# Kernel tuning notes

Hardware: AMD Instinct MI355X
Metric: run time of the kernel (lower is better)

## Reference

```python
import jax, jax.numpy as jnp
import numpy as np

N_ATOMS = 10000
N_EDGES = 150000
NB = 128          # n_atom_basis
NI = 3            # n_interactions
MAX_Z = 100
N_RBF = 20
CUTOFF = 5.0
EPS = 1e-08
BATCH = 64


def setup_inputs() -> dict:
    key = jax.random.key(0)
    ks = jax.random.split(key, 20)
    f32 = jnp.float32
    s = 0.05
    positions = jax.random.normal(ks[0], (N_ATOMS, 3), f32)
    atomic_numbers = jax.random.randint(ks[1], (N_ATOMS,), 0, MAX_Z)
    idx_i = jax.random.randint(ks[2], (N_EDGES,), 0, N_ATOMS)
    off = jax.random.randint(ks[3], (N_EDGES,), 1, N_ATOMS)
    idx_j = (idx_i + off) % N_ATOMS  # avoid self-edges (d_ij == 0)
    idx_m = jnp.sort(jax.random.randint(ks[4], (N_ATOMS,), 0, BATCH))
    emb = (jax.random.normal(ks[5], (MAX_Z, NB), f32) * s).at[0].set(0.0)  # padding_idx=0
    fW = jax.random.normal(ks[6], (N_RBF, NI * 3 * NB), f32) * s
    fb = jnp.zeros((NI * 3 * NB,), f32)
    ic1_W = jax.random.normal(ks[7], (NI, NB, NB), f32) * s
    ic1_b = jnp.zeros((NI, NB), f32)
    ic2_W = jax.random.normal(ks[8], (NI, NB, 3 * NB), f32) * s
    ic2_b = jnp.zeros((NI, 3 * NB), f32)
    mix_W = jax.random.normal(ks[9], (NI, NB, 2 * NB), f32) * s  # no bias
    ctx1_W = jax.random.normal(ks[10], (NI, 2 * NB, NB), f32) * s
    ctx1_b = jnp.zeros((NI, NB), f32)
    ctx2_W = jax.random.normal(ks[11], (NI, NB, 3 * NB), f32) * s
    ctx2_b = jnp.zeros((NI, 3 * NB), f32)
    o1_W = jax.random.normal(ks[12], (NB, NB), f32) * s
    o1_b = jnp.zeros((NB,), f32)
    o2_W = jax.random.normal(ks[13], (NB, NB), f32) * s
    o2_b = jnp.zeros((NB,), f32)
    o3_W = jax.random.normal(ks[14], (NB, 1), f32) * s
    o3_b = jnp.zeros((1,), f32)
    return dict(positions=positions, emb=emb, fW=fW, fb=fb,
                ic1_W=ic1_W, ic1_b=ic1_b, ic2_W=ic2_W, ic2_b=ic2_b,
                mix_W=mix_W, ctx1_W=ctx1_W, ctx1_b=ctx1_b, ctx2_W=ctx2_W, ctx2_b=ctx2_b,
                o1_W=o1_W, o1_b=o1_b, o2_W=o2_W, o2_b=o2_b, o3_W=o3_W, o3_b=o3_b,
                atomic_numbers=atomic_numbers, idx_i=idx_i, idx_j=idx_j, idx_m=idx_m,
                batch_num=BATCH)


def reference(positions, emb, fW, fb, ic1_W, ic1_b, ic2_W, ic2_b,
              mix_W, ctx1_W, ctx1_b, ctx2_W, ctx2_b,
              o1_W, o1_b, o2_W, o2_b, o3_W, o3_b,
              atomic_numbers, idx_i, idx_j, idx_m, batch_num):
    seg = jax.ops.segment_sum
    n_atoms = positions.shape[0]
    # pairwise distances
    r_ij = positions[idx_j] - positions[idx_i]                      # [E,3]
    d_ij = jnp.sqrt(jnp.sum(r_ij * r_ij, axis=-1, keepdims=True))   # [E,1]
    # Gaussian RBF
    offsets = jnp.linspace(0.0, CUTOFF, N_RBF, dtype=positions.dtype)
    width = offsets[1] - offsets[0]
    coeff = -0.5 / (width * width)
    phi = jnp.exp(coeff * (d_ij[..., None] - offsets) ** 2)         # [E,1,20]
    # cosine cutoff
    fcut = (0.5 * (jnp.cos(d_ij * jnp.pi / CUTOFF) + 1.0) * (d_ij < CUTOFF))[..., None]  # [E,1,1]
    filters = (phi @ fW + fb) * fcut                                # [E,1,NI*3*NB]
    dir_ij = r_ij / d_ij                                            # [E,3]
    q = emb[atomic_numbers][:, None]                                # [N,1,NB]
    mu = jnp.zeros((n_atoms, 3, NB), q.dtype)
    for i in range(NI):
        Wij = filters[..., i * 3 * NB:(i + 1) * 3 * NB]             # [E,1,3*NB]
        # interaction
        x = jax.nn.silu(q @ ic1_W[i] + ic1_b[i]) @ ic2_W[i] + ic2_b[i]  # [N,1,3*NB]
        x = Wij * x[idx_j]                                          # [E,1,3*NB]
        dq, dmuR, dmumu = jnp.split(x, 3, axis=-1)                  # [E,1,NB] each
        dq = seg(dq, idx_i, num_segments=n_atoms)                   # [N,1,NB]
        muj = mu[idx_j]                                             # [E,3,NB]
        dmu = dmuR * dir_ij[:, :, None] + dmumu * muj               # [E,3,NB]
        dmu = seg(dmu, idx_i, num_segments=n_atoms)                 # [N,3,NB]
        q = q + dq
        mu = mu + dmu
        # mixing
        mu_mix = mu @ mix_W[i]                                      # [N,3,2*NB]
        mu_V, mu_Wc = jnp.split(mu_mix, 2, axis=-1)                 # [N,3,NB]
        mu_Vn = jnp.sqrt(jnp.sum(mu_V * mu_V, axis=-2, keepdims=True) + EPS)  # [N,1,NB]
        ctx = jnp.concatenate([q, mu_Vn], axis=-1)                  # [N,1,2*NB]
        x = jax.nn.silu(ctx @ ctx1_W[i] + ctx1_b[i]) @ ctx2_W[i] + ctx2_b[i]  # [N,1,3*NB]
        dq_in, dmu_in, dqmu_in = jnp.split(x, 3, axis=-1)
        dmu_in = dmu_in * mu_Wc                                     # [N,3,NB]
        dqmu_in = dqmu_in * jnp.sum(mu_V * mu_Wc, axis=1, keepdims=True)  # [N,1,NB]
        q = q + dq_in + dqmu_in
        mu = mu + dmu_in
    qf = q[:, 0]                                                    # [N,NB]
    h = jax.nn.silu(qf @ o1_W + o1_b)
    h = jax.nn.silu(h @ o2_W + o2_b)
    y = h @ o3_W + o3_b                                             # [N,1]
    y = seg(y, idx_m, num_segments=batch_num)                       # [B,1]
    return (y, mu)
```

## Files before the change

kernel.cpp:

```cpp
#include <hip/hip_runtime.h>
#include <math.h>

#define NA 10000
#define NE 150000
#define NRBF 20
#define CUT 5.0f
#define EPSV 1e-8f
#define NBATCH 64
#define CAP 48
#define PI_F 3.14159265358979323846f

typedef short bf16x8 __attribute__((ext_vector_type(8)));
typedef float f32x4 __attribute__((ext_vector_type(4)));
typedef __fp16 h16x2 __attribute__((ext_vector_type(2)));
typedef unsigned short u16;

__device__ __forceinline__ u16 f2b(float x) {
    unsigned u = __builtin_bit_cast(unsigned, x);
    return (u16)((u + 0x7FFFu + ((u >> 16) & 1u)) >> 16);
}
__device__ __forceinline__ float b2f(u16 b) {
    unsigned u = ((unsigned)b) << 16;
    return __builtin_bit_cast(float, u);
}
__device__ __forceinline__ float silu_f(float x) { return x / (1.0f + expf(-x)); }

#define P_IC1 0
#define P_IC2 49152
#define P_MIX 196608
#define P_C1  294912
#define P_C2  393216
#define P_O1  540672
#define P_O2  557056
#define P_TOT 573440

__global__ __launch_bounds__(64) void pack_k(
    const float* __restrict__ ic1W, const float* __restrict__ ic2W,
    const float* __restrict__ mixW, const float* __restrict__ c1W,
    const float* __restrict__ c2W, const float* __restrict__ o1W,
    const float* __restrict__ o2W, u16* __restrict__ packs) {
    int id = blockIdx.x;
    const float* src; u16* dst; int N, rel;
    if (id < 96)        { int m = id / 32;          rel = id % 32; src = ic1W + m * 16384; dst = packs + P_IC1 + m * 16384; N = 128; }
    else if (id < 384)  { id -= 96;  int m = id / 96; rel = id % 96; src = ic2W + m * 49152; dst = packs + P_IC2 + m * 49152; N = 384; }
    else if (id < 576)  { id -= 384; int m = id / 64; rel = id % 64; src = mixW + m * 32768; dst = packs + P_MIX + m * 32768; N = 256; }
    else if (id < 768)  { id -= 576; int m = id / 64; rel = id % 64; src = c1W  + m * 32768; dst = packs + P_C1  + m * 32768; N = 128; }
    else if (id < 1056) { id -= 768; int m = id / 96; rel = id % 96; src = c2W  + m * 49152; dst = packs + P_C2  + m * 49152; N = 384; }
    else if (id < 1088) { rel = id - 1056; src = o1W; dst = packs + P_O1; N = 128; }
    else                { rel = id - 1088; src = o2W; dst = packs + P_O2; N = 128; }
    int NBT = N >> 4;
    int kb = rel / NBT, nb = rel % NBT;
    int l = threadIdx.x;
    int col = nb * 16 + (l & 15);
    int k0 = kb * 32 + 8 * (l >> 4);
    u16 v[8];
    #pragma unroll
    for (int i = 0; i < 8; i++) v[i] = f2b(src[(size_t)(k0 + i) * N + col]);
    *(bf16x8*)(dst + rel * 512 + l * 8) = *(bf16x8*)v;
}

template<int MT, int K>
__device__ __forceinline__ void stageA(const float* __restrict__ src, int row0,
                                       int maxrow, u16* As) {
    const int NV = MT * K / 4;
    for (int idx = threadIdx.x; idx < NV; idx += 256) {
        int r = idx / (K / 4), c4 = idx % (K / 4);
        float4 v = make_float4(0.f, 0.f, 0.f, 0.f);
        if (row0 + r < maxrow) v = *(const float4*)(src + (size_t)(row0 + r) * K + c4 * 4);
        uint2 o;
        o.x = (unsigned)f2b(v.x) | ((unsigned)f2b(v.y) << 16);
        o.y = (unsigned)f2b(v.z) | ((unsigned)f2b(v.w) << 16);
        *(uint2*)(As + r * (K + 8) + c4 * 4) = o;
    }
}

__device__ __forceinline__ bf16x8 aFrag(const u16* As, int stride, int row, int k0) {
    return *(const bf16x8*)(As + row * stride + k0);
}
__device__ __forceinline__ bf16x8 bFrag(const u16* __restrict__ pack, int NBT,
                                        int ks, int nb, int l) {
    return *(const bf16x8*)(pack + ((size_t)(ks * NBT + nb) * 64 + l) * 8);
}
#define MFMA(a, b, c) __builtin_amdgcn_mfma_f32_16x16x32_bf16(a, b, c, 0, 0, 0)

__global__ void init_q_k(const float* __restrict__ emb, const int* __restrict__ z,
                         float* __restrict__ q) {
    int idx = blockIdx.x * blockDim.x + threadIdx.x;
    if (idx >= NA * 128) return;
    int a = idx >> 7, c = idx & 127;
    q[idx] = emb[z[a] * 128 + c];
}

__global__ void edge_geom_k(const float* __restrict__ pos,
                            const int* __restrict__ idx_i, const int* __restrict__ idx_j,
                            float* __restrict__ edata, int* __restrict__ cnt,
                            int* __restrict__ bucketj) {
    int e = blockIdx.x * blockDim.x + threadIdx.x;
    if (e >= NE) return;
    int i = idx_i[e], j = idx_j[e];
    float rx = pos[j * 3 + 0] - pos[i * 3 + 0];
    float ry = pos[j * 3 + 1] - pos[i * 3 + 1];
    float rz = pos[j * 3 + 2] - pos[i * 3 + 2];
    float d = sqrtf(rx * rx + ry * ry + rz * rz);
    float inv = 1.0f / d;
    float fc = (d < CUT) ? 0.5f * (cosf(d * PI_F / CUT) + 1.0f) : 0.0f;
    const float width = CUT / (float)(NRBF - 1);
    const float coeff = -0.5f / (width * width);
    float ph[NRBF];
    #pragma unroll
    for (int k = 0; k < NRBF; k++) {
        float t = d - (float)k * width;
        ph[k] = expf(coeff * t * t);
    }
    int slot = atomicAdd(&cnt[i], 1);
    if (slot < CAP) {
        bucketj[i * CAP + slot] = j;
        float* ed = edata + ((size_t)i * CAP + slot) * 16;
        ed[0] = rx * inv; ed[1] = ry * inv; ed[2] = rz * inv; ed[3] = fc;
        h16x2* php = (h16x2*)(ed + 4);
        #pragma unroll
        for (int p = 0; p < 10; p++)
            php[p] = __builtin_amdgcn_cvt_pkrtz(ph[2 * p], ph[2 * p + 1]);
    }
}

__global__ void pad_k(int* __restrict__ cnt, int* __restrict__ bucketj,
                      float* __restrict__ edata) {
    int a = blockIdx.x * blockDim.x + threadIdx.x;
    if (a >= NA) return;
    int n = cnt[a]; if (n > CAP) n = CAP;
    int n4 = (n + 3) & ~3;
    for (int k = n; k < n4; k++) {
        bucketj[a * CAP + k] = 0;
        float* ed = edata + ((size_t)a * CAP + k) * 16;
        #pragma unroll
        for (int t = 0; t < 16; t++) ed[t] = 0.f;
    }
    cnt[a] = n4;
}

__global__ __launch_bounds__(256) void mlp1_k(
    const float* __restrict__ q, const u16* __restrict__ pW1, const float* __restrict__ b1,
    const u16* __restrict__ pW2, const float* __restrict__ b2, u16* __restrict__ xmu) {
    __shared__ u16 As[32 * 136];
    __shared__ u16 Hs[32 * 136];
    int abase = blockIdx.x * 32;
    stageA<32, 128>(q, abase, NA, As);
    __syncthreads();
    int l = threadIdx.x & 63, w = threadIdx.x >> 6, lm = l & 15, lg = l >> 4;
    f32x4 acc[2][2];
    #pragma unroll
    for (int j = 0; j < 2; j++)
        #pragma unroll
        for (int mi = 0; mi < 2; mi++) acc[j][mi] = (f32x4){0.f, 0.f, 0.f, 0.f};
    #pragma unroll
    for (int ks = 0; ks < 4; ks++) {
        bf16x8 a0 = aFrag(As, 136, lm, ks * 32 + 8 * lg);
        bf16x8 a1 = aFrag(As, 136, 16 + lm, ks * 32 + 8 * lg);
        #pragma unroll
        for (int j = 0; j < 2; j++) {
            bf16x8 b = bFrag(pW1, 8, ks, w + 4 * j, l);
            acc[j][0] = MFMA(a0, b, acc[j][0]);
            acc[j][1] = MFMA(a1, b, acc[j][1]);
        }
    }
    #pragma unroll
    for (int j = 0; j < 2; j++) {
        int col = 16 * (w + 4 * j) + lm;
        float bb = b1[col];
        #pragma unroll
        for (int mi = 0; mi < 2; mi++)
            #pragma unroll
            for (int v = 0; v < 4; v++)
                Hs[(16 * mi + 4 * lg + v) * 136 + col] = f2b(silu_f(acc[j][mi][v] + bb));
    }
    __syncthreads();
    f32x4 acc2[6][2];
    #pragma unroll
    for (int j = 0; j < 6; j++)
        #pragma unroll
        for (int mi = 0; mi < 2; mi++) acc2[j][mi] = (f32x4){0.f, 0.f, 0.f, 0.f};
    #pragma unroll
    for (int ks = 0; ks < 4; ks++) {
        bf16x8 a0 = aFrag(Hs, 136, lm, ks * 32 + 8 * lg);
        bf16x8 a1 = aFrag(Hs, 136, 16 + lm, ks * 32 + 8 * lg);
        #pragma unroll
        for (int j = 0; j < 6; j++) {
            bf16x8 b = bFrag(pW2, 24, ks, w + 4 * j, l);
            acc2[j][0] = MFMA(a0, b, acc2[j][0]);
            acc2[j][1] = MFMA(a1, b, acc2[j][1]);
        }
    }
    int b = 16 * w + lm;
    #pragma unroll
    for (int mi = 0; mi < 2; mi++)
        #pragma unroll
        for (int v = 0; v < 4; v++) {
            int ga = abase + 16 * mi + 4 * lg + v;
            if (ga >= NA) continue;
            #pragma unroll
            for (int half = 0; half < 2; half++) {
                int c = b + 64 * half;
                float x0 = acc2[half][mi][v]     + b2[c];
                float x1 = acc2[2 + half][mi][v] + b2[128 + c];
                float x2 = acc2[4 + half][mi][v] + b2[256 + c];
                u16* xr = xmu + ((size_t)ga * 128 + c) * 6;
                *(unsigned*)xr = (unsigned)f2b(x0) | ((unsigned)f2b(x1) << 16);
                xr[2] = f2b(x2);
            }
        }
}

template<int IT0>
__global__ __launch_bounds__(128) void gather_k(
    const float* __restrict__ fW, const float* __restrict__ fb,
    const u16* __restrict__ xmu,
    const float* __restrict__ edata, const int* __restrict__ cnt,
    const int* __restrict__ bucketj, int it,
    float* __restrict__ q, float* __restrict__ muF) {
    int a = blockIdx.x;
    int c = threadIdx.x;
    int cb = it * 384;
    h16x2 wp0[10], wp1[10], wp2[10];
    #pragma unroll
    for (int p = 0; p < 10; p++) {
        const float* r0 = fW + (2 * p) * 1152 + cb;
        const float* r1 = fW + (2 * p + 1) * 1152 + cb;
        wp0[p] = __builtin_amdgcn_cvt_pkrtz(r0[c], r1[c]);
        wp1[p] = __builtin_amdgcn_cvt_pkrtz(r0[128 + c], r1[128 + c]);
        if (!IT0) wp2[p] = __builtin_amdgcn_cvt_pkrtz(r0[256 + c], r1[256 + c]);
    }
    float fb0 = fb[cb + c], fb1 = fb[cb + 128 + c];
    float fb2 = IT0 ? 0.f : fb[cb + 256 + c];
    int n4 = cnt[a];
    const int* bj = bucketj + a * CAP;
    const float* eb = edata + (size_t)a * CAP * 16;
    float adq = 0.f, am0 = 0.f, am1 = 0.f, am2 = 0.f;
    for (int e0 = 0; e0 < n4; e0 += 4) {
        int4 j4 = *(const int4*)(bj + e0);
        #pragma unroll
        for (int u = 0; u < 4; u++) {
            int j = __builtin_amdgcn_readfirstlane(
                u == 0 ? j4.x : u == 1 ? j4.y : u == 2 ? j4.z : j4.w);
            const float* ed = eb + (size_t)(e0 + u) * 16;
            const u16* xr = xmu + ((size_t)j * 128 + c) * 6;
            float xc0, xc1, xc2 = 0.f, m0 = 0.f, m1 = 0.f, m2 = 0.f;
            if (IT0) {
                unsigned xv = *(const unsigned*)xr;
                xc0 = b2f((u16)(xv & 0xffff)); xc1 = b2f((u16)(xv >> 16));
            } else {
                uint3 xv = *(const uint3*)xr;
                xc0 = b2f((u16)(xv.x & 0xffff)); xc1 = b2f((u16)(xv.x >> 16));
                xc2 = b2f((u16)(xv.y & 0xffff));
                m0 = b2f((u16)(xv.y >> 16));
                m1 = b2f((u16)(xv.z & 0xffff)); m2 = b2f((u16)(xv.z >> 16));
            }
            float4 gg = *(const float4*)ed;
            const h16x2* php = (const h16x2*)(ed + 4);
            float f0 = fb0, f1 = fb1, f2 = fb2;
            #pragma unroll
            for (int p = 0; p < 10; p++) {
                h16x2 ph = php[p];
                f0 = __builtin_amdgcn_fdot2(ph, wp0[p], f0, false);
                f1 = __builtin_amdgcn_fdot2(ph, wp1[p], f1, false);
                if (!IT0) f2 = __builtin_amdgcn_fdot2(ph, wp2[p], f2, false);
            }
            f0 *= gg.w; f1 *= gg.w;
            float x0 = f0 * xc0, x1 = f1 * xc1;
            adq += x0;
            am0 += x1 * gg.x;
            am1 += x1 * gg.y;
            am2 += x1 * gg.z;
            if (!IT0) {
                f2 *= gg.w;
                float x2 = f2 * xc2;
                am0 += x2 * m0; am1 += x2 * m1; am2 += x2 * m2;
            }
        }
    }
    q[(size_t)a * 128 + c] += adq;
    muF[(size_t)a * 384 + c] += am0;
    muF[(size_t)a * 384 + 128 + c] += am1;
    muF[(size_t)a * 384 + 256 + c] += am2;
}

__global__ __launch_bounds__(256) void mixctx_k(
    float* __restrict__ q, float* __restrict__ muF, u16* __restrict__ xmu,
    const u16* __restrict__ pM,
    const u16* __restrict__ pC1, const float* __restrict__ c1b,
    const u16* __restrict__ pC2, const float* __restrict__ c2b) {
    __shared__ u16 As[48 * 136];
    __shared__ u16 mmL[16 * 768];
    __shared__ u16 Cs[16 * 264];
    __shared__ u16 Hs[16 * 136];
    int abase = blockIdx.x * 16;
    stageA<48, 128>(muF, abase * 3, 3 * NA, As);
    __syncthreads();
    int l = threadIdx.x & 63, w = threadIdx.x >> 6, lm = l & 15, lg = l >> 4;
    {
        f32x4 acc[4][3];
        #pragma unroll
        for (int j = 0; j < 4; j++)
            #pragma unroll
            for (int mi = 0; mi < 3; mi++) acc[j][mi] = (f32x4){0.f, 0.f, 0.f, 0.f};
        #pragma unroll
        for (int ks = 0; ks < 4; ks++) {
            bf16x8 a[3];
            #pragma unroll
            for (int mi = 0; mi < 3; mi++) a[mi] = aFrag(As, 136, 16 * mi + lm, ks * 32 + 8 * lg);
            #pragma unroll
            for (int j = 0; j < 4; j++) {
                bf16x8 b = bFrag(pM, 16, ks, w + 4 * j, l);
                #pragma unroll
                for (int mi = 0; mi < 3; mi++) acc[j][mi] = MFMA(a[mi], b, acc[j][mi]);
            }
        }
        #pragma unroll
        for (int j = 0; j < 4; j++) {
            int col = 16 * (w + 4 * j) + lm;
            #pragma unroll
            for (int mi = 0; mi < 3; mi++)
                #pragma unroll
                for (int v = 0; v < 4; v++) {
                    int R = 16 * mi + 4 * lg + v;
                    mmL[(R / 3) * 768 + (R % 3) * 256 + col] = f2b(acc[j][mi][v]);
                }
        }
    }
    __syncthreads();
    for (int idx = threadIdx.x; idx < 16 * 128; idx += 256) {
        int a = idx >> 7, cc = idx & 127;
        int ga = abase + a;
        float s = EPSV;
        #pragma unroll
        for (int d = 0; d < 3; d++) {
            float t = b2f(mmL[a * 768 + d * 256 + cc]);
            s += t * t;
        }
        float qv = (ga < NA) ? q[(size_t)ga * 128 + cc] : 0.f;
        Cs[a * 264 + cc] = f2b(qv);
        Cs[a * 264 + 128 + cc] = f2b(sqrtf(s));
    }
    __syncthreads();
    {
        f32x4 h[2];
        h[0] = (f32x4){0.f, 0.f, 0.f, 0.f}; h[1] = (f32x4){0.f, 0.f, 0.f, 0.f};
        #pragma unroll
        for (int ks = 0; ks < 8; ks++) {
            bf16x8 a0 = aFrag(Cs, 264, lm, ks * 32 + 8 * lg);
            #pragma unroll
            for (int j = 0; j < 2; j++) {
                bf16x8 b = bFrag(pC1, 8, ks, w + 4 * j, l);
                h[j] = MFMA(a0, b, h[j]);
            }
        }
        #pragma unroll
        for (int j = 0; j < 2; j++) {
            int col = 16 * (w + 4 * j) + lm;
            float bb = c1b[col];
            #pragma unroll
            for (int v = 0; v < 4; v++)
                Hs[(4 * lg + v) * 136 + col] = f2b(silu_f(h[j][v] + bb));
        }
    }
    __syncthreads();
    f32x4 acc2[6];
    #pragma unroll
    for (int j = 0; j < 6; j++) acc2[j] = (f32x4){0.f, 0.f, 0.f, 0.f};
    #pragma unroll
    for (int ks = 0; ks < 4; ks++) {
        bf16x8 a0 = aFrag(Hs, 136, lm, ks * 32 + 8 * lg);
        #pragma unroll
        for (int j = 0; j < 6; j++) {
            bf16x8 b = bFrag(pC2, 24, ks, w + 4 * j, l);
            acc2[j] = MFMA(a0, b, acc2[j]);
        }
    }
    #pragma unroll
    for (int j = 0; j < 6; j++) {
        float bb = c2b[16 * (w + 4 * j) + lm];
        #pragma unroll
        for (int v = 0; v < 4; v++) acc2[j][v] += bb;
    }
    #pragma unroll
    for (int v = 0; v < 4; v++) {
        int al = 4 * lg + v;
        int ga = abase + al;
        if (ga >= NA) continue;
        #pragma unroll
        for (int jj = 0; jj < 2; jj++) {
            int cc = 16 * w + 64 * jj + lm;
            float x0 = acc2[jj][v], x1 = acc2[jj + 2][v], x2 = acc2[jj + 4][v];
            float dot = 0.f, muW[3], mnew[3];
            #pragma unroll
            for (int d = 0; d < 3; d++) {
                float muV = b2f(mmL[al * 768 + d * 256 + cc]);
                muW[d] = b2f(mmL[al * 768 + d * 256 + 128 + cc]);
                dot += muV * muW[d];
            }
            q[(size_t)ga * 128 + cc] += x0 + x2 * dot;
            #pragma unroll
            for (int d = 0; d < 3; d++) {
                size_t mo = (size_t)ga * 384 + d * 128 + cc;
                float m = muF[mo] + x1 * muW[d];
                muF[mo] = m;
                mnew[d] = m;
            }
            u16* xr = xmu + ((size_t)ga * 128 + cc) * 6;
            xr[3] = f2b(mnew[0]);
            *(unsigned*)(xr + 4) = (unsigned)f2b(mnew[1]) | ((unsigned)f2b(mnew[2]) << 16);
        }
    }
}

__global__ __launch_bounds__(256) void readout_k(
    const float* __restrict__ q, const u16* __restrict__ pO1, const float* __restrict__ o1b,
    const u16* __restrict__ pO2, const float* __restrict__ o2b,
    const float* __restrict__ o3W, const float* __restrict__ o3b,
    const int* __restrict__ idx_m, float* __restrict__ y) {
    __shared__ u16 As[32 * 136];
    __shared__ u16 Hs[32 * 136];
    __shared__ float red[256];
    __shared__ float part[NBATCH];
    __shared__ int mlo, mhi;
    int abase = blockIdx.x * 32;
    stageA<32, 128>(q, abase, NA, As);
    __syncthreads();
    int l = threadIdx.x & 63, w = threadIdx.x >> 6, lm = l & 15, lg = l >> 4;
    f32x4 acc[2][2];
    #pragma unroll
    for (int j = 0; j < 2; j++)
        #pragma unroll
        for (int mi = 0; mi < 2; mi++) acc[j][mi] = (f32x4){0.f, 0.f, 0.f, 0.f};
    #pragma unroll
    for (int ks = 0; ks < 4; ks++) {
        bf16x8 a0 = aFrag(As, 136, lm, ks * 32 + 8 * lg);
        bf16x8 a1 = aFrag(As, 136, 16 + lm, ks * 32 + 8 * lg);
        #pragma unroll
        for (int j = 0; j < 2; j++) {
            bf16x8 b = bFrag(pO1, 8, ks, w + 4 * j, l);
            acc[j][0] = MFMA(a0, b, acc[j][0]);
            acc[j][1] = MFMA(a1, b, acc[j][1]);
        }
    }
    #pragma unroll
    for (int j = 0; j < 2; j++) {
        int col = 16 * (w + 4 * j) + lm;
        float bb = o1b[col];
        #pragma unroll
        for (int mi = 0; mi < 2; mi++)
            #pragma unroll
            for (int v = 0; v < 4; v++)
                Hs[(16 * mi + 4 * lg + v) * 136 + col] = f2b(silu_f(acc[j][mi][v] + bb));
    }
    __syncthreads();
    f32x4 acc2[2][2];
    #pragma unroll
    for (int j = 0; j < 2; j++)
        #pragma unroll
        for (int mi = 0; mi < 2; mi++) acc2[j][mi] = (f32x4){0.f, 0.f, 0.f, 0.f};
    #pragma unroll
    for (int ks = 0; ks < 4; ks++) {
        bf16x8 a0 = aFrag(Hs, 136, lm, ks * 32 + 8 * lg);
        bf16x8 a1 = aFrag(Hs, 136, 16 + lm, ks * 32 + 8 * lg);
        #pragma unroll
        for (int j = 0; j < 2; j++) {
            bf16x8 b = bFrag(pO2, 8, ks, w + 4 * j, l);
            acc2[j][0] = MFMA(a0, b, acc2[j][0]);
            acc2[j][1] = MFMA(a1, b, acc2[j][1]);
        }
    }
    #pragma unroll
    for (int j = 0; j < 2; j++) {
        int col = 16 * (w + 4 * j) + lm;
        float bb = o2b[col];
        #pragma unroll
        for (int mi = 0; mi < 2; mi++)
            #pragma unroll
            for (int v = 0; v < 4; v++)
                As[(16 * mi + 4 * lg + v) * 136 + col] = f2b(silu_f(acc2[j][mi][v] + bb));
    }
    if (threadIdx.x < NBATCH) part[threadIdx.x] = 0.f;
    if (threadIdx.x == 0) { mlo = NBATCH; mhi = -1; }
    __syncthreads();
    int a = threadIdx.x >> 3, gseg = threadIdx.x & 7;
    float p = 0.f;
    #pragma unroll
    for (int cc = 0; cc < 16; cc++) {
        int c = gseg * 16 + cc;
        p += b2f(As[a * 136 + c]) * o3W[c];
    }
    red[threadIdx.x] = p;
    __syncthreads();
    if (gseg == 0) {
        float s = 0.f;
        #pragma unroll
        for (int k = 0; k < 8; k++) s += red[a * 8 + k];
        int ga = abase + a;
        if (ga < NA) {
            int m = idx_m[ga];
            atomicAdd(&part[m], s + o3b[0]);
            atomicMin(&mlo, m);
            atomicMax(&mhi, m);
        }
    }
    __syncthreads();
    for (int m = mlo + (int)threadIdx.x; m <= mhi; m += 256)
        atomicAdd(&y[m], part[m]);
}

extern "C" void kernel_launch(void* const* d_in, const int* in_sizes, int n_in,
                              void* d_out, int out_size, void* d_ws, size_t ws_size,
                              hipStream_t stream) {
    const float* pos  = (const float*)d_in[0];
    const float* emb  = (const float*)d_in[1];
    const float* fW   = (const float*)d_in[2];
    const float* fb   = (const float*)d_in[3];
    const float* ic1W = (const float*)d_in[4];
    const float* ic1b = (const float*)d_in[5];
    const float* ic2W = (const float*)d_in[6];
    const float* ic2b = (const float*)d_in[7];
    const float* mixW = (const float*)d_in[8];
    const float* c1W  = (const float*)d_in[9];
    const float* c1b  = (const float*)d_in[10];
    const float* c2W  = (const float*)d_in[11];
    const float* c2b  = (const float*)d_in[12];
    const float* o1W  = (const float*)d_in[13];
    const float* o1b  = (const float*)d_in[14];
    const float* o2W  = (const float*)d_in[15];
    const float* o2b  = (const float*)d_in[16];
    const float* o3W  = (const float*)d_in[17];
    const float* o3b  = (const float*)d_in[18];
    const int* zn     = (const int*)d_in[19];
    const int* idx_i  = (const int*)d_in[20];
    const int* idx_j  = (const int*)d_in[21];
    const int* idx_m  = (const int*)d_in[22];

    float* y   = (float*)d_out;
    float* muF = (float*)d_out + NBATCH;

    char* wp = (char*)d_ws;
    float* q      = (float*)wp;  wp += (size_t)NA * 128 * 4;
    u16*   xmu    = (u16*)wp;    wp += (size_t)NA * 128 * 6 * 2;
    float* edata  = (float*)wp;  wp += (size_t)NA * CAP * 16 * 4;
    int*   cnt    = (int*)wp;    wp += (size_t)NA * 4;
    int*   bucketj= (int*)wp;    wp += (size_t)NA * CAP * 4;
    u16*   packs  = (u16*)wp;    wp += (size_t)P_TOT * 2;

    hipMemsetAsync(d_out, 0, (size_t)(NBATCH + (size_t)NA * 384) * 4, stream);
    hipMemsetAsync(cnt, 0, (size_t)NA * 4, stream);

    pack_k<<<1120, 64, 0, stream>>>(ic1W, ic2W, mixW, c1W, c2W, o1W, o2W, packs);
    init_q_k<<<(NA * 128 + 255) / 256, 256, 0, stream>>>(emb, zn, q);
    edge_geom_k<<<(NE + 255) / 256, 256, 0, stream>>>(pos, idx_i, idx_j, edata, cnt, bucketj);
    pad_k<<<(NA + 255) / 256, 256, 0, stream>>>(cnt, bucketj, edata);

    for (int it = 0; it < 3; it++) {
        mlp1_k<<<313, 256, 0, stream>>>(
            q, packs + P_IC1 + it * 16384, ic1b + it * 128,
            packs + P_IC2 + it * 49152, ic2b + it * 384, xmu);
        if (it == 0)
            gather_k<1><<<NA, 128, 0, stream>>>(
                fW, fb, xmu, edata, cnt, bucketj, it, q, muF);
        else
            gather_k<0><<<NA, 128, 0, stream>>>(
                fW, fb, xmu, edata, cnt, bucketj, it, q, muF);
        mixctx_k<<<(NA + 15) / 16, 256, 0, stream>>>(
            q, muF, xmu,
            packs + P_MIX + it * 32768,
            packs + P_C1 + it * 32768, c1b + it * 128,
            packs + P_C2 + it * 49152, c2b + it * 384);
    }

    readout_k<<<313, 256, 0, stream>>>(q, packs + P_O1, o1b, packs + P_O2, o2b,
                                       o3W, o3b, idx_m, y);
}
```

Measured before the change: 395.9 us.

## Fuse next-iteration interaction MLP into mixctx kernel and prepack filter weights as fp16

The mixing/context kernel now also runs the next iteration's interaction MLP (ic1/ic2) on the freshly updated q held in shared memory. This removes two separate mlp1 launches and a reload of q from global memory. The filter weights fW are also converted once to packed fp16 pairs in pack_k, so gather_k loads pre-converted halves instead of converting per block. The cost is extra shared memory and registers in the fused kernel, which may lower occupancy.

Measured after the change: 407.6 us. 3.0% more time.

```diff
diff --git a/kernel.cpp b/kernel.cpp
--- a/kernel.cpp
+++ b/kernel.cpp
@@ -32,14 +32,27 @@
 #define P_C2  393216
 #define P_O1  540672
 #define P_O2  557056
-#define P_TOT 573440
+#define P_FWH 573440
+#define P_TOT 596480
 
 __global__ __launch_bounds__(64) void pack_k(
     const float* __restrict__ ic1W, const float* __restrict__ ic2W,
     const float* __restrict__ mixW, const float* __restrict__ c1W,
     const float* __restrict__ c2W, const float* __restrict__ o1W,
-    const float* __restrict__ o2W, u16* __restrict__ packs) {
+    const float* __restrict__ o2W, const float* __restrict__ fW,
+    u16* __restrict__ packs) {
     int id = blockIdx.x;
+    if (id >= 1120) {
+        int col = (id - 1120) * 64 + (int)threadIdx.x;
+        unsigned* dst32 = (unsigned*)(packs + P_FWH);
+        #pragma unroll
+        for (int p = 0; p < 10; p++) {
+            h16x2 v = __builtin_amdgcn_cvt_pkrtz(fW[(size_t)(2 * p) * 1152 + col],
+                                                 fW[(size_t)(2 * p + 1) * 1152 + col]);
+            dst32[p * 1152 + col] = __builtin_bit_cast(unsigned, v);
+        }
+        return;
+    }
     const float* src; u16* dst; int N, rel;
     if (id < 96)        { int m = id / 32;          rel = id % 32; src = ic1W + m * 16384; dst = packs + P_IC1 + m * 16384; N = 128; }
     else if (id < 384)  { id -= 96;  int m = id / 96; rel = id % 96; src = ic2W + m * 49152; dst = packs + P_IC2 + m * 49152; N = 384; }
@@ -213,7 +226,7 @@
 
 template<int IT0>
 __global__ __launch_bounds__(128) void gather_k(
-    const float* __restrict__ fW, const float* __restrict__ fb,
+    const unsigned* __restrict__ fWh, const float* __restrict__ fb,
     const u16* __restrict__ xmu,
     const float* __restrict__ edata, const int* __restrict__ cnt,
     const int* __restrict__ bucketj, int it,
@@ -224,11 +237,9 @@
     h16x2 wp0[10], wp1[10], wp2[10];
     #pragma unroll
     for (int p = 0; p < 10; p++) {
-        const float* r0 = fW + (2 * p) * 1152 + cb;
-        const float* r1 = fW + (2 * p + 1) * 1152 + cb;
-        wp0[p] = __builtin_amdgcn_cvt_pkrtz(r0[c], r1[c]);
-        wp1[p] = __builtin_amdgcn_cvt_pkrtz(r0[128 + c], r1[128 + c]);
-        if (!IT0) wp2[p] = __builtin_amdgcn_cvt_pkrtz(r0[256 + c], r1[256 + c]);
+        wp0[p] = __builtin_bit_cast(h16x2, fWh[p * 1152 + cb + c]);
+        wp1[p] = __builtin_bit_cast(h16x2, fWh[p * 1152 + cb + 128 + c]);
+        if (!IT0) wp2[p] = __builtin_bit_cast(h16x2, fWh[p * 1152 + cb + 256 + c]);
     }
     float fb0 = fb[cb + c], fb1 = fb[cb + 128 + c];
     float fb2 = IT0 ? 0.f : fb[cb + 256 + c];
@@ -284,15 +295,19 @@
     muF[(size_t)a * 384 + 256 + c] += am2;
 }
 
-__global__ __launch_bounds__(256) void mixctx_k(
+template<int DO_MLP>
+__global__ __launch_bounds__(256) void mixmlp_k(
     float* __restrict__ q, float* __restrict__ muF, u16* __restrict__ xmu,
     const u16* __restrict__ pM,
     const u16* __restrict__ pC1, const float* __restrict__ c1b,
-    const u16* __restrict__ pC2, const float* __restrict__ c2b) {
+    const u16* __restrict__ pC2, const float* __restrict__ c2b,
+    const u16* __restrict__ pW1, const float* __restrict__ b1,
+    const u16* __restrict__ pW2, const float* __restrict__ b2) {
     __shared__ u16 As[48 * 136];
     __shared__ u16 mmL[16 * 768];
     __shared__ u16 Cs[16 * 264];
     __shared__ u16 Hs[16 * 136];
+    __shared__ u16 Qs[16 * 136];
     int abase = blockIdx.x * 16;
     stageA<48, 128>(muF, abase * 3, 3 * NA, As);
     __syncthreads();
@@ -398,7 +413,10 @@
                 muW[d] = b2f(mmL[al * 768 + d * 256 + 128 + cc]);
                 dot += muV * muW[d];
             }
-            q[(size_t)ga * 128 + cc] += x0 + x2 * dot;
+            float qold = q[(size_t)ga * 128 + cc];
+            float qnew = qold + x0 + x2 * dot;
+            q[(size_t)ga * 128 + cc] = qnew;
+            if (DO_MLP) Qs[al * 136 + cc] = f2b(qnew);
             #pragma unroll
             for (int d = 0; d < 3; d++) {
                 size_t mo = (size_t)ga * 384 + d * 128 + cc;
@@ -409,6 +427,58 @@
             u16* xr = xmu + ((size_t)ga * 128 + cc) * 6;
             xr[3] = f2b(mnew[0]);
             *(unsigned*)(xr + 4) = (unsigned)f2b(mnew[1]) | ((unsigned)f2b(mnew[2]) << 16);
+        }
+    }
+    if (!DO_MLP) return;
+    __syncthreads();
+    {
+        f32x4 h[2];
+        h[0] = (f32x4){0.f, 0.f, 0.f, 0.f}; h[1] = (f32x4){0.f, 0.f, 0.f, 0.f};
+        #pragma unroll
+        for (int ks = 0; ks < 4; ks++) {
+            bf16x8 a0 = aFrag(Qs, 136, lm, ks * 32 + 8 * lg);
+            #pragma unroll
+            for (int j = 0; j < 2; j++) {
+                bf16x8 b = bFrag(pW1, 8, ks, w + 4 * j, l);
+                h[j] = MFMA(a0, b, h[j]);
+            }
+        }
+        #pragma unroll
+        for (int j = 0; j < 2; j++) {
+            int col = 16 * (w + 4 * j) + lm;
+            float bb = b1[col];
+            #pragma unroll
+            for (int v = 0; v < 4; v++)
+                Hs[(4 * lg + v) * 136 + col] = f2b(silu_f(h[j][v] + bb));
+        }
+    }
+    __syncthreads();
+    f32x4 acc3[6];
+    #pragma unroll
+    for (int j = 0; j < 6; j++) acc3[j] = (f32x4){0.f, 0.f, 0.f, 0.f};
+    #pragma unroll
+    for (int ks = 0; ks < 4; ks++) {
+        bf16x8 a0 = aFrag(Hs, 136, lm, ks * 32 + 8 * lg);
+        #pragma unroll
+        for (int j = 0; j < 6; j++) {
+            bf16x8 b = bFrag(pW2, 24, ks, w + 4 * j, l);
+            acc3[j] = MFMA(a0, b, acc3[j]);
+        }
+    }
+    int b = 16 * w + lm;
+    #pragma unroll
+    for (int v = 0; v < 4; v++) {
+        int ga = abase + 4 * lg + v;
+        if (ga >= NA) continue;
+        #pragma unroll
+        for (int half = 0; half < 2; half++) {
+            int cx = b + 64 * half;
+            float x0 = acc3[half][v]     + b2[cx];
+            float x1 = acc3[2 + half][v] + b2[128 + cx];
+            float x2 = acc3[4 + half][v] + b2[256 + cx];
+            u16* xr = xmu + ((size_t)ga * 128 + cx) * 6;
+            *(unsigned*)xr = (unsigned)f2b(x0) | ((unsigned)f2b(x1) << 16);
+            xr[2] = f2b(x2);
         }
     }
 }
@@ -550,26 +620,38 @@
     hipMemsetAsync(d_out, 0, (size_t)(NBATCH + (size_t)NA * 384) * 4, stream);
     hipMemsetAsync(cnt, 0, (size_t)NA * 4, stream);
 
-    pack_k<<<1120, 64, 0, stream>>>(ic1W, ic2W, mixW, c1W, c2W, o1W, o2W, packs);
+    pack_k<<<1138, 64, 0, stream>>>(ic1W, ic2W, mixW, c1W, c2W, o1W, o2W, fW, packs);
     init_q_k<<<(NA * 128 + 255) / 256, 256, 0, stream>>>(emb, zn, q);
     edge_geom_k<<<(NE + 255) / 256, 256, 0, stream>>>(pos, idx_i, idx_j, edata, cnt, bucketj);
     pad_k<<<(NA + 255) / 256, 256, 0, stream>>>(cnt, bucketj, edata);
 
+    const unsigned* fWh = (const unsigned*)(packs + P_FWH);
+
+    mlp1_k<<<313, 256, 0, stream>>>(
+        q, packs + P_IC1, ic1b, packs + P_IC2, ic2b, xmu);
+
     for (int it = 0; it < 3; it++) {
-        mlp1_k<<<313, 256, 0, stream>>>(
-            q, packs + P_IC1 + it * 16384, ic1b + it * 128,
-            packs + P_IC2 + it * 49152, ic2b + it * 384, xmu);
         if (it == 0)
             gather_k<1><<<NA, 128, 0, stream>>>(
-                fW, fb, xmu, edata, cnt, bucketj, it, q, muF);
+                fWh, fb, xmu, edata, cnt, bucketj, it, q, muF);
         else
             gather_k<0><<<NA, 128, 0, stream>>>(
-                fW, fb, xmu, edata, cnt, bucketj, it, q, muF);
-        mixctx_k<<<(NA + 15) / 16, 256, 0, stream>>>(
-            q, muF, xmu,
-            packs + P_MIX + it * 32768,
-            packs + P_C1 + it * 32768, c1b + it * 128,
-            packs + P_C2 + it * 49152, c2b + it * 384);
+                fWh, fb, xmu, edata, cnt, bucketj, it, q, muF);
+        if (it < 2)
+            mixmlp_k<1><<<(NA + 15) / 16, 256, 0, stream>>>(
+                q, muF, xmu,
+                packs + P_MIX + it * 32768,
+                packs + P_C1 + it * 32768, c1b + it * 128,
+                packs + P_C2 + it * 49152, c2b + it * 384,
+                packs + P_IC1 + (it + 1) * 16384, ic1b + (it + 1) * 128,
+                packs + P_IC2 + (it + 1) * 49152, ic2b + (it + 1) * 384);
+        else
+            mixmlp_k<0><<<(NA + 15) / 16, 256, 0, stream>>>(
+                q, muF, xmu,
+                packs + P_MIX + it * 32768,
+                packs + P_C1 + it * 32768, c1b + it * 128,
+                packs + P_C2 + it * 49152, c2b + it * 384,
+                packs + P_IC1, ic1b, packs + P_IC2, ic2b);
     }
 
     readout_k<<<313, 256, 0, stream>>>(q, packs + P_O1, o1b, packs + P_O2, o2b,
```
